# Kernel tuning notes

Measured on AMD Instinct MI355X. Metric: run time of the kernel, lower is better.

Reference implementation:

```python
import jax, jax.numpy as jnp
import numpy as np

B, T, C, H = 4, 2048, 768, 12
D = C // H

def setup_inputs() -> dict:
    key = jax.random.key(0)
    ks = jax.random.split(key, 8)
    s = 1.0 / np.sqrt(C)
    return {
        "x":  jax.random.normal(ks[0], (B, T, C), dtype=jnp.float32),
        "Wq": jax.random.normal(ks[1], (C, C), dtype=jnp.float32) * s,
        "bq": jax.random.normal(ks[2], (C,), dtype=jnp.float32) * 0.02,
        "Wk": jax.random.normal(ks[3], (C, C), dtype=jnp.float32) * s,
        "bk": jax.random.normal(ks[4], (C,), dtype=jnp.float32) * 0.02,
        "Wv": jax.random.normal(ks[5], (C, C), dtype=jnp.float32) * s,
        "bv": jax.random.normal(ks[6], (C,), dtype=jnp.float32) * 0.02,
        "Wp": jax.random.normal(ks[7], (C, C), dtype=jnp.float32) * s,
    }

def reference(x, Wq, bq, Wk, bk, Wv, bv, Wp):
    # Linear projections (torch Linear: y = x @ W.T + b)
    q = x @ Wq.T + bq
    k = x @ Wk.T + bk
    v = x @ Wv.T + bv
    # [B,T,C] -> [B,H,T,D]
    q = q.reshape(B, T, H, D).transpose(0, 2, 1, 3)
    k = k.reshape(B, T, H, D).transpose(0, 2, 1, 3)
    v = v.reshape(B, T, H, D).transpose(0, 2, 1, 3)
    scale = 1.0 / np.sqrt(D).astype(np.float32)
    scores = jnp.einsum('bhqd,bhkd->bhqk', q, k) * scale  # [B,H,T,T]
    attn = jax.nn.softmax(scores, axis=-1)  # no mask in original module
    out = jnp.einsum('bhqk,bhkd->bhqd', attn, v)
    out = out.transpose(0, 2, 1, 3).reshape(B, T, C)
    return out @ Wp.T  # proj has bias=False
```

## Files before the change

kernel.cpp:

```cpp
#include <hip/hip_runtime.h>
#include <hip/hip_bf16.h>
#include <cmath>

constexpr int B  = 4;
constexpr int T  = 2048;
constexpr int C  = 768;
constexpr int H  = 12;
constexpr int Dh = 64;
constexpr int M  = B * T;
constexpr int NQKV = 3 * C;
constexpr int WS2  = C * C;

typedef short bf16x8 __attribute__((ext_vector_type(8)));
typedef short bf16x4 __attribute__((ext_vector_type(4)));
typedef float f32x4  __attribute__((ext_vector_type(4)));

__device__ inline short f2bf(float f) {
    unsigned u = __float_as_uint(f);
    u += 0x7fffu + ((u >> 16) & 1u);
    return (short)(u >> 16);
}

__device__ inline unsigned pk_bf16(float a, float b) {
    __hip_bfloat162 h = __float22bfloat162_rn(float2{a, b});
    return *(unsigned*)&h;
}

typedef const __attribute__((address_space(1))) unsigned GU;
typedef __attribute__((address_space(3))) unsigned LU;
__device__ inline void async_copy16(const void* g, void* l) {
    __builtin_amdgcn_global_load_lds((GU*)g, (LU*)l, 16, 0, 0);
}

__global__ __launch_bounds__(256)
void convert_x(const float* __restrict__ src, short* __restrict__ dst) {
    size_t i = ((size_t)blockIdx.x * 256 + threadIdx.x) * 4;
    float4 v = *(const float4*)(src + i);
    bf16x4 o; o[0] = f2bf(v.x); o[1] = f2bf(v.y); o[2] = f2bf(v.z); o[3] = f2bf(v.w);
    *(bf16x4*)(dst + i) = o;
}

__global__ __launch_bounds__(256)
void convert_weights(const float* __restrict__ Wq, const float* __restrict__ Wk,
                     const float* __restrict__ Wv, const float* __restrict__ Wp,
                     short* __restrict__ Wqkv, short* __restrict__ Wpb) {
    const float* src; short* dst;
    switch (blockIdx.y) {
        case 0:  src = Wq; dst = Wqkv;           break;
        case 1:  src = Wk; dst = Wqkv + WS2;     break;
        case 2:  src = Wv; dst = Wqkv + 2 * WS2; break;
        default: src = Wp; dst = Wpb;            break;
    }
    size_t i = ((size_t)blockIdx.x * 256 + threadIdx.x) * 4;
    float4 v = *(const float4*)(src + i);
    bf16x4 o; o[0] = f2bf(v.x); o[1] = f2bf(v.y); o[2] = f2bf(v.z); o[3] = f2bf(v.w);
    *(bf16x4*)(dst + i) = o;
}

constexpr int BM = 128, BN = 128, BK = 32;

template<int OUT_BF16>
__global__ __launch_bounds__(256)
void gemm_bt(const short* __restrict__ A, const short* __restrict__ W,
             const float* __restrict__ bias0, const float* __restrict__ bias1,
             const float* __restrict__ bias2,
             void* __restrict__ Yv, int Ndim, int Kdim) {
    __shared__ short As[BM * BK];
    __shared__ short Bs[BN * BK];

    const int tid  = threadIdx.x;
    const int wave = tid >> 6;
    const int lane = tid & 63;
    const int li   = lane & 15;
    const int quad = lane >> 4;
    const int wm   = wave >> 1;
    const int wn   = wave & 1;
    const int m0   = blockIdx.y * BM;
    const int n0   = blockIdx.x * BN;

    f32x4 acc[4][4];
    #pragma unroll
    for (int i = 0; i < 4; ++i)
        #pragma unroll
        for (int j = 0; j < 4; ++j)
            acc[i][j] = (f32x4){0.f, 0.f, 0.f, 0.f};

    const int lrow = lane >> 2;
    const int lkof = (lane & 3) * 8;

    for (int k0 = 0; k0 < Kdim; k0 += BK) {
        __syncthreads();
        #pragma unroll
        for (int i = 0; i < 2; ++i) {
            int c = wave * 2 + i;
            int row = c * 16 + lrow;
            async_copy16(A + (size_t)(m0 + row) * Kdim + k0 + lkof, &As[c * 512]);
            async_copy16(W + (size_t)(n0 + row) * Kdim + k0 + lkof, &Bs[c * 512]);
        }
        __syncthreads();

        bf16x8 af[4], bfr[4];
        #pragma unroll
        for (int t = 0; t < 4; ++t) {
            af[t]  = *(const bf16x8*)&As[(wm * 64 + t * 16 + li) * BK + quad * 8];
            bfr[t] = *(const bf16x8*)&Bs[(wn * 64 + t * 16 + li) * BK + quad * 8];
        }
        #pragma unroll
        for (int i = 0; i < 4; ++i)
            #pragma unroll
            for (int j = 0; j < 4; ++j)
                acc[i][j] = __builtin_amdgcn_mfma_f32_16x16x32_bf16(
                    af[i], bfr[j], acc[i][j], 0, 0, 0);
    }

    float bb[4] = {0.f, 0.f, 0.f, 0.f};
    if (bias0) {
        int s = n0 / C;
        const float* bp = (s == 0) ? bias0 : ((s == 1) ? bias1 : bias2);
        int nb = n0 % C;
        #pragma unroll
        for (int nt = 0; nt < 4; ++nt)
            bb[nt] = bp[nb + wn * 64 + nt * 16 + li];
    }

    #pragma unroll
    for (int mt = 0; mt < 4; ++mt)
        #pragma unroll
        for (int nt = 0; nt < 4; ++nt)
            #pragma unroll
            for (int r = 0; r < 4; ++r) {
                int row = m0 + wm * 64 + mt * 16 + quad * 4 + r;
                int col = n0 + wn * 64 + nt * 16 + li;
                float v = acc[mt][nt][r] + bb[nt];
                if constexpr (OUT_BF16)
                    ((short*)Yv)[(size_t)row * Ndim + col] = f2bf(v);
                else
                    ((float*)Yv)[(size_t)row * Ndim + col] = v;
            }
}

constexpr int QT   = 128;
constexpr int KTT  = 64;
constexpr int LSTR = 72;
constexpr int PSTR = 72;
constexpr int QS   = NQKV;
constexpr float SOFT_SCALE = 0.18033688011112042f;

__global__ __launch_bounds__(256)
void attn_fwd(const short* __restrict__ QKV, short* __restrict__ O) {
    __shared__ short Ks[KTT * LSTR];
    __shared__ short Vt[Dh * LSTR];
    __shared__ short Ps[4 * 32 * PSTR];

    const int tid  = threadIdx.x;
    const int wave = tid >> 6;
    const int lane = tid & 63;
    const int li   = lane & 15;
    const int quad = lane >> 4;
    const int b    = blockIdx.z;
    const int h    = blockIdx.y;
    const int qw   = blockIdx.x * QT + wave * 32;

    const short* Qg = QKV + (size_t)(b * T) * QS + h * Dh;
    const short* Kg = QKV + (size_t)(b * T) * QS + C + h * Dh;
    const short* Vg = QKV + (size_t)(b * T) * QS + 2 * C + h * Dh;

    bf16x8 qf[2][2];
    #pragma unroll
    for (int qb = 0; qb < 2; ++qb)
        #pragma unroll
        for (int dh = 0; dh < 2; ++dh)
            qf[qb][dh] = *(const bf16x8*)(Qg + (size_t)(qw + qb * 16 + li) * QS
                                             + dh * 32 + quad * 8);

    bf16x8 ones;
    #pragma unroll
    for (int i = 0; i < 8; ++i) ones[i] = (short)0x3F80;

    f32x4 oacc[2][4];
    #pragma unroll
    for (int qb = 0; qb < 2; ++qb)
        #pragma unroll
        for (int db = 0; db < 4; ++db)
            oacc[qb][db] = (f32x4){0.f, 0.f, 0.f, 0.f};
    f32x4 lacc[2] = {(f32x4){0.f, 0.f, 0.f, 0.f}, (f32x4){0.f, 0.f, 0.f, 0.f}};

    const int vd2 = (tid & 31) * 2;
    const int vg  = tid >> 5;

    for (int kt = 0; kt < T; kt += KTT) {
        __syncthreads();
        #pragma unroll
        for (int i = 0; i < 2; ++i) {
            int idx = i * 256 + tid;
            int tok = idx >> 3, ch = idx & 7;
            *(int4*)&Ks[tok * LSTR + ch * 8] =
                *(const int4*)(Kg + (size_t)(kt + tok) * QS + ch * 8);
        }
        {
            bf16x8 vlo, vhi;
            #pragma unroll
            for (int t2 = 0; t2 < 8; ++t2) {
                unsigned u = *(const unsigned*)(Vg + (size_t)(kt + vg * 8 + t2) * QS + vd2);
                vlo[t2] = (short)(u & 0xffffu);
                vhi[t2] = (short)(u >> 16);
            }
            *(bf16x8*)&Vt[vd2 * LSTR + vg * 8]       = vlo;
            *(bf16x8*)&Vt[(vd2 + 1) * LSTR + vg * 8] = vhi;
        }
        __syncthreads();

        f32x4 st[2][4];
        #pragma unroll
        for (int kb = 0; kb < 4; ++kb) {
            bf16x8 kf0 = *(const bf16x8*)&Ks[(kb * 16 + li) * LSTR + quad * 8];
            bf16x8 kf1 = *(const bf16x8*)&Ks[(kb * 16 + li) * LSTR + 32 + quad * 8];
            #pragma unroll
            for (int qb = 0; qb < 2; ++qb) {
                f32x4 a = (f32x4){0.f, 0.f, 0.f, 0.f};
                a = __builtin_amdgcn_mfma_f32_16x16x32_bf16(kf0, qf[qb][0], a, 0, 0, 0);
                a = __builtin_amdgcn_mfma_f32_16x16x32_bf16(kf1, qf[qb][1], a, 0, 0, 0);
                st[qb][kb] = a;
            }
        }

        #pragma unroll
        for (int qb = 0; qb < 2; ++qb)
            #pragma unroll
            for (int kb = 0; kb < 4; ++kb) {
                float p0 = exp2f(st[qb][kb][0] * SOFT_SCALE);
                float p1 = exp2f(st[qb][kb][1] * SOFT_SCALE);
                float p2 = exp2f(st[qb][kb][2] * SOFT_SCALE);
                float p3 = exp2f(st[qb][kb][3] * SOFT_SCALE);
                uint2 w; w.x = pk_bf16(p0, p1); w.y = pk_bf16(p2, p3);
                *(uint2*)&Ps[(wave * 32 + qb * 16 + li) * PSTR + kb * 16 + quad * 4] = w;
            }
        __asm__ volatile("s_waitcnt lgkmcnt(0)" ::: "memory");

        #pragma unroll
        for (int kq = 0; kq < 2; ++kq) {
            bf16x8 pf[2];
            #pragma unroll
            for (int qb = 0; qb < 2; ++qb) {
                pf[qb] = *(const bf16x8*)&Ps[(wave * 32 + qb * 16 + li) * PSTR
                                             + kq * 32 + quad * 8];
                lacc[qb] = __builtin_amdgcn_mfma_f32_16x16x32_bf16(
                    pf[qb], ones, lacc[qb], 0, 0, 0);
            }
            #pragma unroll
            for (int db = 0; db < 4; ++db) {
                bf16x8 vf = *(const bf16x8*)&Vt[(db * 16 + li) * LSTR + kq * 32 + quad * 8];
                #pragma unroll
                for (int qb = 0; qb < 2; ++qb)
                    oacc[qb][db] = __builtin_amdgcn_mfma_f32_16x16x32_bf16(
                        pf[qb], vf, oacc[qb][db], 0, 0, 0);
            }
        }
    }

    #pragma unroll
    for (int qb = 0; qb < 2; ++qb)
        #pragma unroll
        for (int r = 0; r < 4; ++r) {
            float inv = 1.0f / lacc[qb][r];
            short* op = O + (size_t)(b * T + qw + qb * 16 + quad * 4 + r) * C
                          + h * Dh + li;
            #pragma unroll
            for (int db = 0; db < 4; ++db)
                op[db * 16] = f2bf(oacc[qb][db][r] * inv);
        }
}

extern "C" void kernel_launch(void* const* d_in, const int* in_sizes, int n_in,
                              void* d_out, int out_size, void* d_ws, size_t ws_size,
                              hipStream_t stream) {
    (void)in_sizes; (void)n_in; (void)out_size; (void)ws_size;

    const float* x  = (const float*)d_in[0];
    const float* Wq = (const float*)d_in[1];
    const float* bq = (const float*)d_in[2];
    const float* Wk = (const float*)d_in[3];
    const float* bk = (const float*)d_in[4];
    const float* Wv = (const float*)d_in[5];
    const float* bv = (const float*)d_in[6];
    const float* Wp = (const float*)d_in[7];
    float* out = (float*)d_out;

    short* xb    = (short*)d_ws;
    short* Wqkv  = xb + (size_t)M * C;
    short* Wpb   = Wqkv + 3 * (size_t)WS2;
    short* QKVb  = Wpb + (size_t)WS2;
    short* AOb   = QKVb + (size_t)M * NQKV;

    convert_x<<<dim3((M * C) / 1024), 256, 0, stream>>>(x, xb);
    convert_weights<<<dim3(WS2 / 1024, 4), 256, 0, stream>>>(Wq, Wk, Wv, Wp, Wqkv, Wpb);

    gemm_bt<1><<<dim3(NQKV / BN, M / BM), 256, 0, stream>>>(
        xb, Wqkv, bq, bk, bv, QKVb, NQKV, C);

    attn_fwd<<<dim3(T / QT, H, B), 256, 0, stream>>>(QKVb, AOb);

    gemm_bt<0><<<dim3(C / BN, M / BM), 256, 0, stream>>>(
        AOb, Wpb, nullptr, nullptr, nullptr, out, C, C);
}
```

Before: 268.5 us.

## Merge convert kernels, template GEMM tiles, prefetch V and read K directly

Result: slower. 283.8 us (+5.7%).

```diff
diff --git a/kernel.cpp b/kernel.cpp
--- a/kernel.cpp
+++ b/kernel.cpp
@@ -32,57 +32,56 @@
     __builtin_amdgcn_global_load_lds((GU*)g, (LU*)l, 16, 0, 0);
 }
 
+constexpr size_t XE = (size_t)M * C;
+constexpr size_t CV_TOTAL = XE + 4 * (size_t)WS2;
+
 __global__ __launch_bounds__(256)
-void convert_x(const float* __restrict__ src, short* __restrict__ dst) {
+void convert_all(const float* __restrict__ x,  const float* __restrict__ Wq,
+                 const float* __restrict__ Wk, const float* __restrict__ Wv,
+                 const float* __restrict__ Wp,
+                 short* __restrict__ xb, short* __restrict__ Wqkv,
+                 short* __restrict__ Wpb) {
     size_t i = ((size_t)blockIdx.x * 256 + threadIdx.x) * 4;
-    float4 v = *(const float4*)(src + i);
+    const float* src; short* dst; size_t off;
+    if (i < XE)                    { src = x;  dst = xb;            off = i; }
+    else if (i < XE + WS2)         { src = Wq; dst = Wqkv;          off = i - XE; }
+    else if (i < XE + 2 * (size_t)WS2) { src = Wk; dst = Wqkv + WS2;     off = i - XE - WS2; }
+    else if (i < XE + 3 * (size_t)WS2) { src = Wv; dst = Wqkv + 2 * WS2; off = i - XE - 2 * (size_t)WS2; }
+    else                           { src = Wp; dst = Wpb;           off = i - XE - 3 * (size_t)WS2; }
+    float4 v = *(const float4*)(src + off);
     bf16x4 o; o[0] = f2bf(v.x); o[1] = f2bf(v.y); o[2] = f2bf(v.z); o[3] = f2bf(v.w);
-    *(bf16x4*)(dst + i) = o;
-}
-
-__global__ __launch_bounds__(256)
-void convert_weights(const float* __restrict__ Wq, const float* __restrict__ Wk,
-                     const float* __restrict__ Wv, const float* __restrict__ Wp,
-                     short* __restrict__ Wqkv, short* __restrict__ Wpb) {
-    const float* src; short* dst;
-    switch (blockIdx.y) {
-        case 0:  src = Wq; dst = Wqkv;           break;
-        case 1:  src = Wk; dst = Wqkv + WS2;     break;
-        case 2:  src = Wv; dst = Wqkv + 2 * WS2; break;
-        default: src = Wp; dst = Wpb;            break;
-    }
-    size_t i = ((size_t)blockIdx.x * 256 + threadIdx.x) * 4;
-    float4 v = *(const float4*)(src + i);
-    bf16x4 o; o[0] = f2bf(v.x); o[1] = f2bf(v.y); o[2] = f2bf(v.z); o[3] = f2bf(v.w);
-    *(bf16x4*)(dst + i) = o;
-}
-
-constexpr int BM = 128, BN = 128, BK = 32;
-
-template<int OUT_BF16>
+    *(bf16x4*)(dst + off) = o;
+}
+
+constexpr int BM = 128, BK = 32;
+
+template<int BN_, int WMW, int WNW, int OUT_BF16>
 __global__ __launch_bounds__(256)
 void gemm_bt(const short* __restrict__ A, const short* __restrict__ W,
              const float* __restrict__ bias0, const float* __restrict__ bias1,
              const float* __restrict__ bias2,
              void* __restrict__ Yv, int Ndim, int Kdim) {
+    constexpr int MT = BM / WMW / 16;
+    constexpr int NT = BN_ / WNW / 16;
+    constexpr int NCHUNK = (BM + BN_) / 16;
     __shared__ short As[BM * BK];
-    __shared__ short Bs[BN * BK];
+    __shared__ short Bs[BN_ * BK];
 
     const int tid  = threadIdx.x;
     const int wave = tid >> 6;
     const int lane = tid & 63;
     const int li   = lane & 15;
     const int quad = lane >> 4;
-    const int wm   = wave >> 1;
-    const int wn   = wave & 1;
+    const int wm   = wave % WMW;
+    const int wn   = wave / WMW;
     const int m0   = blockIdx.y * BM;
-    const int n0   = blockIdx.x * BN;
-
-    f32x4 acc[4][4];
-    #pragma unroll
-    for (int i = 0; i < 4; ++i)
-        #pragma unroll
-        for (int j = 0; j < 4; ++j)
+    const int n0   = blockIdx.x * BN_;
+
+    f32x4 acc[MT][NT];
+    #pragma unroll
+    for (int i = 0; i < MT; ++i)
+        #pragma unroll
+        for (int j = 0; j < NT; ++j)
             acc[i][j] = (f32x4){0.f, 0.f, 0.f, 0.f};
 
     const int lrow = lane >> 2;
@@ -91,46 +90,52 @@
     for (int k0 = 0; k0 < Kdim; k0 += BK) {
         __syncthreads();
         #pragma unroll
-        for (int i = 0; i < 2; ++i) {
-            int c = wave * 2 + i;
-            int row = c * 16 + lrow;
-            async_copy16(A + (size_t)(m0 + row) * Kdim + k0 + lkof, &As[c * 512]);
-            async_copy16(W + (size_t)(n0 + row) * Kdim + k0 + lkof, &Bs[c * 512]);
+        for (int ii = 0; ii < NCHUNK / 4; ++ii) {
+            int c = ii * 4 + wave;
+            if (c < BM / 16)
+                async_copy16(A + (size_t)(m0 + c * 16 + lrow) * Kdim + k0 + lkof,
+                             &As[c * 512]);
+            else
+                async_copy16(W + (size_t)(n0 + (c - BM / 16) * 16 + lrow) * Kdim + k0 + lkof,
+                             &Bs[(c - BM / 16) * 512]);
         }
         __syncthreads();
 
-        bf16x8 af[4], bfr[4];
-        #pragma unroll
-        for (int t = 0; t < 4; ++t) {
-            af[t]  = *(const bf16x8*)&As[(wm * 64 + t * 16 + li) * BK + quad * 8];
-            bfr[t] = *(const bf16x8*)&Bs[(wn * 64 + t * 16 + li) * BK + quad * 8];
-        }
-        #pragma unroll
-        for (int i = 0; i < 4; ++i)
-            #pragma unroll
-            for (int j = 0; j < 4; ++j)
+        bf16x8 af[MT], bfr[NT];
+        #pragma unroll
+        for (int t = 0; t < MT; ++t)
+            af[t] = *(const bf16x8*)&As[(wm * MT * 16 + t * 16 + li) * BK + quad * 8];
+        #pragma unroll
+        for (int t = 0; t < NT; ++t)
+            bfr[t] = *(const bf16x8*)&Bs[(wn * NT * 16 + t * 16 + li) * BK + quad * 8];
+        #pragma unroll
+        for (int i = 0; i < MT; ++i)
+            #pragma unroll
+            for (int j = 0; j < NT; ++j)
                 acc[i][j] = __builtin_amdgcn_mfma_f32_16x16x32_bf16(
                     af[i], bfr[j], acc[i][j], 0, 0, 0);
     }
 
-    float bb[4] = {0.f, 0.f, 0.f, 0.f};
+    float bb[NT];
+    #pragma unroll
+    for (int nt = 0; nt < NT; ++nt) bb[nt] = 0.f;
     if (bias0) {
         int s = n0 / C;
         const float* bp = (s == 0) ? bias0 : ((s == 1) ? bias1 : bias2);
         int nb = n0 % C;
         #pragma unroll
-        for (int nt = 0; nt < 4; ++nt)
-            bb[nt] = bp[nb + wn * 64 + nt * 16 + li];
+        for (int nt = 0; nt < NT; ++nt)
+            bb[nt] = bp[nb + wn * NT * 16 + nt * 16 + li];
     }
 
     #pragma unroll
-    for (int mt = 0; mt < 4; ++mt)
-        #pragma unroll
-        for (int nt = 0; nt < 4; ++nt)
+    for (int mt = 0; mt < MT; ++mt)
+        #pragma unroll
+        for (int nt = 0; nt < NT; ++nt)
             #pragma unroll
             for (int r = 0; r < 4; ++r) {
-                int row = m0 + wm * 64 + mt * 16 + quad * 4 + r;
-                int col = n0 + wn * 64 + nt * 16 + li;
+                int row = m0 + wm * MT * 16 + mt * 16 + quad * 4 + r;
+                int col = n0 + wn * NT * 16 + nt * 16 + li;
                 float v = acc[mt][nt][r] + bb[nt];
                 if constexpr (OUT_BF16)
                     ((short*)Yv)[(size_t)row * Ndim + col] = f2bf(v);
@@ -148,8 +153,7 @@
 
 __global__ __launch_bounds__(256)
 void attn_fwd(const short* __restrict__ QKV, short* __restrict__ O) {
-    __shared__ short Ks[KTT * LSTR];
-    __shared__ short Vt[Dh * LSTR];
+    __shared__ short Vt[2][Dh * LSTR];
     __shared__ short Ps[4 * 32 * PSTR];
 
     const int tid  = threadIdx.x;
@@ -188,33 +192,38 @@
     const int vd2 = (tid & 31) * 2;
     const int vg  = tid >> 5;
 
+    unsigned vpre[8];
+    #pragma unroll
+    for (int t2 = 0; t2 < 8; ++t2)
+        vpre[t2] = *(const unsigned*)(Vg + (size_t)(vg * 8 + t2) * QS + vd2);
+
     for (int kt = 0; kt < T; kt += KTT) {
-        __syncthreads();
-        #pragma unroll
-        for (int i = 0; i < 2; ++i) {
-            int idx = i * 256 + tid;
-            int tok = idx >> 3, ch = idx & 7;
-            *(int4*)&Ks[tok * LSTR + ch * 8] =
-                *(const int4*)(Kg + (size_t)(kt + tok) * QS + ch * 8);
-        }
+        const int p = (kt >> 6) & 1;
+
         {
             bf16x8 vlo, vhi;
             #pragma unroll
             for (int t2 = 0; t2 < 8; ++t2) {
-                unsigned u = *(const unsigned*)(Vg + (size_t)(kt + vg * 8 + t2) * QS + vd2);
-                vlo[t2] = (short)(u & 0xffffu);
-                vhi[t2] = (short)(u >> 16);
-            }
-            *(bf16x8*)&Vt[vd2 * LSTR + vg * 8]       = vlo;
-            *(bf16x8*)&Vt[(vd2 + 1) * LSTR + vg * 8] = vhi;
+                vlo[t2] = (short)(vpre[t2] & 0xffffu);
+                vhi[t2] = (short)(vpre[t2] >> 16);
+            }
+            *(bf16x8*)&Vt[p][vd2 * LSTR + vg * 8]       = vlo;
+            *(bf16x8*)&Vt[p][(vd2 + 1) * LSTR + vg * 8] = vhi;
         }
         __syncthreads();
 
+        if (kt + KTT < T) {
+            #pragma unroll
+            for (int t2 = 0; t2 < 8; ++t2)
+                vpre[t2] = *(const unsigned*)(Vg + (size_t)(kt + KTT + vg * 8 + t2) * QS + vd2);
+        }
+
         f32x4 st[2][4];
         #pragma unroll
         for (int kb = 0; kb < 4; ++kb) {
-            bf16x8 kf0 = *(const bf16x8*)&Ks[(kb * 16 + li) * LSTR + quad * 8];
-            bf16x8 kf1 = *(const bf16x8*)&Ks[(kb * 16 + li) * LSTR + 32 + quad * 8];
+            const short* kr = Kg + (size_t)(kt + kb * 16 + li) * QS + quad * 8;
+            bf16x8 kf0 = *(const bf16x8*)kr;
+            bf16x8 kf1 = *(const bf16x8*)(kr + 32);
             #pragma unroll
             for (int qb = 0; qb < 2; ++qb) {
                 f32x4 a = (f32x4){0.f, 0.f, 0.f, 0.f};
@@ -249,7 +258,7 @@
             }
             #pragma unroll
             for (int db = 0; db < 4; ++db) {
-                bf16x8 vf = *(const bf16x8*)&Vt[(db * 16 + li) * LSTR + kq * 32 + quad * 8];
+                bf16x8 vf = *(const bf16x8*)&Vt[p][(db * 16 + li) * LSTR + kq * 32 + quad * 8];
                 #pragma unroll
                 for (int qb = 0; qb < 2; ++qb)
                     oacc[qb][db] = __builtin_amdgcn_mfma_f32_16x16x32_bf16(
@@ -292,14 +301,14 @@
     short* QKVb  = Wpb + (size_t)WS2;
     short* AOb   = QKVb + (size_t)M * NQKV;
 
-    convert_x<<<dim3((M * C) / 1024), 256, 0, stream>>>(x, xb);
-    convert_weights<<<dim3(WS2 / 1024, 4), 256, 0, stream>>>(Wq, Wk, Wv, Wp, Wqkv, Wpb);
-
-    gemm_bt<1><<<dim3(NQKV / BN, M / BM), 256, 0, stream>>>(
+    convert_all<<<dim3(CV_TOTAL / 1024), 256, 0, stream>>>(
+        x, Wq, Wk, Wv, Wp, xb, Wqkv, Wpb);
+
+    gemm_bt<128, 2, 2, 1><<<dim3(NQKV / 128, M / BM), 256, 0, stream>>>(
         xb, Wqkv, bq, bk, bv, QKVb, NQKV, C);
 
     attn_fwd<<<dim3(T / QT, H, B), 256, 0, stream>>>(QKVb, AOb);
 
-    gemm_bt<0><<<dim3(C / BN, M / BM), 256, 0, stream>>>(
+    gemm_bt<64, 4, 1, 0><<<dim3(C / 64, M / BM), 256, 0, stream>>>(
         AOb, Wpb, nullptr, nullptr, nullptr, out, C, C);
 }
```
